# Performance work log

Measured on AMD Instinct MI355X. Metric: run time of the kernel, lower is better.

Reference implementation:

```python
import jax, jax.numpy as jnp
import numpy as np

EPS = 1e-12  # matches torch F.normalize eps
TEMPERATURE = 1.0
LAMBDA = 0.8


def _l2norm(x):
    n = jnp.sqrt(jnp.sum(x * x, axis=-1, keepdims=True))
    return x / jnp.maximum(n, EPS)


def setup_inputs() -> dict:
    key = jax.random.key(0)
    feats = jax.random.normal(key, (4, 4096, 512), dtype=jnp.float32)
    return {"feats": feats, "node": 8}


def reference(feats, node):
    f = _l2norm(feats)                                   # [B,N,D]
    scores = jnp.einsum('bnd,bmd->bnm', f, f) / TEMPERATURE  # [B,N,N]
    vals, idx = jax.lax.top_k(scores, node)              # [B,N,k]
    B, N, _ = scores.shape
    bi = jnp.arange(B)[:, None, None]
    ni = jnp.arange(N)[None, :, None]
    sparse = jnp.full_like(scores, -jnp.inf).at[bi, ni, idx].set(vals)
    w = jax.nn.softmax(sparse, axis=-1)                  # zeros outside top-k
    feats_att = jnp.einsum('bnm,bmd->bnd', w, f)
    feats_gam = f * LAMBDA + feats_att * (1.0 - LAMBDA)
    return _l2norm(feats_gam)
```

## Files before the change

### kernel.cpp

```cpp
#include <hip/hip_runtime.h>
#include <stdint.h>

#define NROWS 4096
#define NDIM  512
#define TOPT  8
#define NLIST 16
#define NCAND 128
#define NRESC 12
#define KSEL  8

typedef __attribute__((ext_vector_type(8))) short short8;
typedef __attribute__((ext_vector_type(4))) float f32x4;

__device__ __forceinline__ unsigned short f2bf(float x) {
  unsigned int u = __float_as_uint(x);
  return (unsigned short)((u + 0x7fffu + ((u >> 16) & 1u)) >> 16);
}

__device__ __forceinline__ void gl_lds16(const void* g, void* l) {
  void* gnc = (void*)g;
  __builtin_amdgcn_global_load_lds(
      (__attribute__((address_space(1))) void*)gnc,
      (__attribute__((address_space(3))) void*)l, 16, 0, 0);
}

__device__ __forceinline__ void ins8(unsigned int (&tv)[TOPT], unsigned int k) {
#pragma unroll
  for (int j = 0; j < TOPT; ++j) {
    const unsigned int nt = tv[j] > k ? tv[j] : k;
    k = tv[j] > k ? k : tv[j];
    tv[j] = nt;
  }
}

__global__ __launch_bounds__(256) void k_norm(const float* __restrict__ in,
                                              float* __restrict__ fout,
                                              unsigned short* __restrict__ fbf) {
  const int row = blockIdx.x * 4 + (threadIdx.x >> 6);
  const int l = threadIdx.x & 63;
  const float4* src = reinterpret_cast<const float4*>(in + (size_t)row * NDIM);
  float4 a = src[l * 2], b = src[l * 2 + 1];
  float ss = a.x * a.x + a.y * a.y + a.z * a.z + a.w * a.w +
             b.x * b.x + b.y * b.y + b.z * b.z + b.w * b.w;
#pragma unroll
  for (int off = 32; off; off >>= 1) ss += __shfl_xor(ss, off, 64);
  const float inv = 1.0f / fmaxf(sqrtf(ss), 1e-12f);
  a.x *= inv; a.y *= inv; a.z *= inv; a.w *= inv;
  b.x *= inv; b.y *= inv; b.z *= inv; b.w *= inv;
  float4* dst = reinterpret_cast<float4*>(fout + (size_t)row * NDIM);
  dst[l * 2] = a; dst[l * 2 + 1] = b;
  uint4 ub;
  ub.x = (unsigned)f2bf(a.x) | ((unsigned)f2bf(a.y) << 16);
  ub.y = (unsigned)f2bf(a.z) | ((unsigned)f2bf(a.w) << 16);
  ub.z = (unsigned)f2bf(b.x) | ((unsigned)f2bf(b.y) << 16);
  ub.w = (unsigned)f2bf(b.z) | ((unsigned)f2bf(b.w) << 16);
  reinterpret_cast<uint4*>(fbf + (size_t)row * NDIM)[l] = ub;
}

__global__ __launch_bounds__(512, 4) void k_coarse(const unsigned short* __restrict__ fbf,
                                                   unsigned int* __restrict__ keys) {
  __shared__ alignas(16) union {
    struct { unsigned short A[128 * 64]; unsigned short B[128 * 64]; } st;
    unsigned short S[128 * 128];
  } sh;

  const int tid = threadIdx.x;
  const int w = tid >> 6, l = tid & 63;

  const int lin = blockIdx.x;
  const int xcd = lin & 7;
  const int slot = lin >> 3;
  const int xq = xcd * 4 + (slot & 3);
  const int ym = (slot >> 2) & 7;
  const int zb = slot >> 5;

  const int q0 = xq * 128;
  const int m0 = ym * 512;
  const int bbase = zb * NROWS;

  const int qh = w >> 2, mq = w & 3;
  const int r = tid >> 2, sub = tid & 3;
  const int rx = r & 31;

  const int lrow = (l >> 3);
  const int lkg  = ((l & 7) ^ lrow) * 8;

  unsigned int tv[TOPT];
#pragma unroll
  for (int j = 0; j < TOPT; ++j) tv[j] = 0u;

  const f32x4 vzero = {0.f, 0.f, 0.f, 0.f};

  for (int mt = 0; mt < 4; ++mt) {
    const int mbase = m0 + mt * 128;
    f32x4 acc[4][2];
#pragma unroll
    for (int i = 0; i < 4; ++i)
#pragma unroll
      for (int j = 0; j < 2; ++j) acc[i][j] = vzero;

    for (int kt = 0; kt < 8; ++kt) {
      const int kk = kt * 64;
#pragma unroll
      for (int t = 0; t < 2; ++t) {
        const int sa = w * 2 + t;
        const int srow = sa * 8 + lrow;
        gl_lds16(fbf + ((size_t)(bbase + q0 + srow) << 9) + kk + lkg,
                 &sh.st.A[sa * 512]);
        gl_lds16(fbf + ((size_t)(bbase + mbase + srow) << 9) + kk + lkg,
                 &sh.st.B[sa * 512]);
      }
      __syncthreads();
#pragma unroll
      for (int ks = 0; ks < 2; ++ks) {
        short8 av[4], bv[2];
        const int kgrp = ks * 4 + (l >> 4);
#pragma unroll
        for (int i = 0; i < 4; ++i) {
          const int row = qh * 64 + i * 16 + (l & 15);
          av[i] = *(const short8*)&sh.st.A[row * 64 + (kgrp ^ (l & 7)) * 8];
        }
#pragma unroll
        for (int j = 0; j < 2; ++j) {
          const int row = mq * 32 + j * 16 + (l & 15);
          bv[j] = *(const short8*)&sh.st.B[row * 64 + (kgrp ^ (l & 7)) * 8];
        }
#pragma unroll
        for (int i = 0; i < 4; ++i)
#pragma unroll
          for (int j = 0; j < 2; ++j)
            acc[i][j] = __builtin_amdgcn_mfma_f32_16x16x32_bf16(av[i], bv[j], acc[i][j], 0, 0, 0);
      }
      __syncthreads();
    }

#pragma unroll
    for (int i = 0; i < 4; ++i) {
      const int qb_ = qh * 64 + i * 16 + (l >> 4) * 4;
#pragma unroll
      for (int j = 0; j < 2; ++j) {
        const int mc = mq * 32 + j * 16 + (l & 15);
#pragma unroll
        for (int rr = 0; rr < 4; ++rr) {
          const int q = qb_ + rr;
          unsigned int uu = __float_as_uint(acc[i][j][rr]);
          uu ^= (unsigned int)(((int)uu) >> 31) | 0x80000000u;
          const int pg = ((mc >> 2) ^ (q & 31));
          sh.S[q * 128 + pg * 4 + (mc & 3)] = (unsigned short)(uu >> 16);
        }
      }
    }
    __syncthreads();

    {
      const int invb0 = 4095 - (mbase + sub * 32);
#pragma unroll 4
      for (int cg = 0; cg < 8; ++cg) {
        const int pg = (sub * 8 + cg) ^ rx;
        const ushort4 s4 = *(const ushort4*)&sh.S[r * 128 + pg * 4];
        const unsigned int invb = (unsigned int)(invb0 - cg * 4);
        const unsigned int k0 = ((unsigned int)s4.x << 16) | invb;
        const unsigned int k1 = ((unsigned int)s4.y << 16) | (invb - 1);
        const unsigned int k2 = ((unsigned int)s4.z << 16) | (invb - 2);
        const unsigned int k3 = ((unsigned int)s4.w << 16) | (invb - 3);
        if (k0 > tv[TOPT - 1]) ins8(tv, k0);
        if (k1 > tv[TOPT - 1]) ins8(tv, k1);
        if (k2 > tv[TOPT - 1]) ins8(tv, k2);
        if (k3 > tv[TOPT - 1]) ins8(tv, k3);
      }
    }
    __syncthreads();
  }

  unsigned int ov[TOPT];
#pragma unroll
  for (int j = 0; j < TOPT; ++j) ov[j] = __shfl_xor(tv[j], 1, 64);
  unsigned int mg[TOPT];
#pragma unroll
  for (int j = 0; j < TOPT; ++j) {
    const unsigned int o = ov[TOPT - 1 - j];
    mg[j] = tv[j] > o ? tv[j] : o;
  }

  if ((sub & 1) == 0) {
    const int list = ym * 2 + (sub >> 1);
    unsigned int* dst = keys + (((size_t)(bbase + q0 + r)) * NLIST + list) * TOPT;
    reinterpret_cast<uint4*>(dst)[0] = make_uint4(mg[0], mg[1], mg[2], mg[3]);
    reinterpret_cast<uint4*>(dst)[1] = make_uint4(mg[4], mg[5], mg[6], mg[7]);
  }
}

__global__ __launch_bounds__(256) void k_sel(const float* __restrict__ f,
                                             const unsigned int* __restrict__ keys,
                                             uint2* __restrict__ selw) {
  __shared__ int sh_si[4][NRESC];

  const int lin = blockIdx.x;
  const int xcd = lin & 7;
  const int slot = lin >> 3;
  const int b = xcd >> 1;
  const int wv = threadIdx.x >> 6;
  const int n = ((xcd & 1) * 512 + slot) * 4 + wv;
  const int qg = b * NROWS + n;
  const int l = threadIdx.x & 63;

  const uint2 kk = reinterpret_cast<const uint2*>(keys + (size_t)qg * NCAND)[l];
  const unsigned int ka = kk.x, kb = kk.y;

  unsigned int T = 0u;
#pragma unroll
  for (int bit = 31; bit >= 0; --bit) {
    const unsigned int Tp = T | (1u << bit);
    const int cnt = (int)__popcll(__ballot(ka >= Tp)) +
                    (int)__popcll(__ballot(kb >= Tp));
    T = (cnt >= NRESC) ? Tp : T;
  }

  {
    const unsigned long long mA = __ballot(ka >= T);
    const unsigned long long mB = __ballot(kb >= T);
    const unsigned long long lt = (1ull << l) - 1ull;
    if (ka >= T) sh_si[wv][(int)__popcll(mA & lt)] = 4095 - (int)(ka & 4095u);
    if (kb >= T) sh_si[wv][(int)__popcll(mA) + (int)__popcll(mB & lt)] =
        4095 - (int)(kb & 4095u);
  }
  asm volatile("s_waitcnt lgkmcnt(0)" ::: "memory");
  __builtin_amdgcn_sched_barrier(0);

  int si[NRESC];
#pragma unroll
  for (int j = 0; j < NRESC; ++j)
    si[j] = __builtin_amdgcn_readfirstlane(sh_si[wv][j]);

  const float* __restrict__ fb = f + (size_t)b * NROWS * NDIM;
  const float* frow = fb + (size_t)n * NDIM;
  float selfv[8];
#pragma unroll
  for (int c = 0; c < 8; ++c) selfv[c] = frow[c * 64 + l];

  double ex[NRESC];
#pragma unroll
  for (int rr = 0; rr < NRESC; ++rr) {
    const float* g = fb + (size_t)si[rr] * NDIM;
    double s = 0.0;
#pragma unroll
    for (int c = 0; c < 8; ++c) s += (double)selfv[c] * (double)g[c * 64 + l];
    ex[rr] = s;
  }
#pragma unroll
  for (int off = 32; off; off >>= 1) {
#pragma unroll
    for (int rr = 0; rr < NRESC; ++rr) ex[rr] += __shfl_xor(ex[rr], off, 64);
  }

  unsigned mask = 0;
  double wex[KSEL]; int wi[KSEL];
#pragma unroll
  for (int rr = 0; rr < KSEL; ++rr) {
    double mv = -1.0e300; int midx = 0x7fffffff; int mslot = 0;
#pragma unroll
    for (int j = 0; j < NRESC; ++j) {
      const bool avail = ((mask >> j) & 1u) == 0u;
      if (avail && (ex[j] > mv || (ex[j] == mv && si[j] < midx))) {
        mv = ex[j]; midx = si[j]; mslot = j;
      }
    }
    mask |= 1u << mslot;
    wex[rr] = mv; wi[rr] = midx;
  }

  float w8[KSEL];
  const float mx = (float)wex[0];
  float wsum = 0.f;
#pragma unroll
  for (int rr = 0; rr < KSEL; ++rr) { w8[rr] = expf((float)wex[rr] - mx); wsum += w8[rr]; }
  const float cs = 0.2f / wsum;

  uint2 osel = make_uint2(0u, 0u);
#pragma unroll
  for (int rr = 0; rr < KSEL; ++rr) {
    if (l == rr) osel = make_uint2((unsigned)wi[rr], __float_as_uint(cs * w8[rr]));
  }
  if (l < KSEL) selw[(size_t)qg * KSEL + l] = osel;
}

__global__ __launch_bounds__(256) void k_blend(const float* __restrict__ f,
                                               const uint2* __restrict__ selw,
                                               float* __restrict__ out) {
  const int row = blockIdx.x * 4 + (threadIdx.x >> 6);
  const int b = row >> 12;
  const int l = threadIdx.x & 63;

  const uint2* pw = selw + (size_t)row * KSEL;
  uint2 p[KSEL];
#pragma unroll
  for (int j = 0; j < KSEL; ++j) p[j] = pw[j];

  const float* __restrict__ fb = f + (size_t)b * NROWS * NDIM;
  const float* frow = f + (size_t)row * NDIM;

  float acc[8];
#pragma unroll
  for (int c = 0; c < 8; ++c) acc[c] = 0.8f * frow[c * 64 + l];
#pragma unroll
  for (int j = 0; j < KSEL; ++j) {
    const float* g = fb + (size_t)p[j].x * NDIM;
    const float wr = __uint_as_float(p[j].y);
#pragma unroll
    for (int c = 0; c < 8; ++c) acc[c] = fmaf(wr, g[c * 64 + l], acc[c]);
  }

  float ss = 0.f;
#pragma unroll
  for (int c = 0; c < 8; ++c) ss += acc[c] * acc[c];
#pragma unroll
  for (int off = 32; off; off >>= 1) ss += __shfl_xor(ss, off, 64);
  const float inv = 1.0f / fmaxf(sqrtf(ss), 1e-12f);
  float* orow = out + (size_t)row * NDIM;
#pragma unroll
  for (int c = 0; c < 8; ++c) orow[c * 64 + l] = acc[c] * inv;
}

extern "C" void kernel_launch(void* const* d_in, const int* in_sizes, int n_in,
                              void* d_out, int out_size, void* d_ws, size_t ws_size,
                              hipStream_t stream) {
  (void)in_sizes; (void)n_in; (void)out_size; (void)ws_size;
  const float* feats = (const float*)d_in[0];
  char* ws = (char*)d_ws;
  float*          fnorm = (float*)(ws);
  unsigned short* fbf   = (unsigned short*)(ws + 33554432);
  unsigned int*   keys  = (unsigned int*)(ws + 50331648);
  uint2*          selw  = (uint2*)(ws + 58720256);
  float* out = (float*)d_out;

  k_norm <<<dim3(4096), dim3(256), 0, stream>>>(feats, fnorm, fbf);
  k_coarse<<<dim3(1024), dim3(512), 0, stream>>>(fbf, keys);
  k_sel  <<<dim3(4096), dim3(256), 0, stream>>>(fnorm, keys, selw);
  k_blend<<<dim3(4096), dim3(256), 0, stream>>>(fnorm, selw, out);
}
```

Measured before the change: 278.9 us.

## Exploit Gram symmetry: compute upper-triangle tiles only and drop fp32 normalized copy

The coarse scoring kernel now computes only the upper-triangular 128x128 tiles of each batch's symmetric similarity matrix. Each tile emits top-8 candidates for both its row block and its column block, using a transposed LDS copy, and diagonal tiles load a single operand. This roughly halves the bf16 MFMA work, but candidate lists double to 32 per row, so the selection kernel reads and radix-filters 256 keys instead of 128. The fp32 normalized feature buffer is also removed: later kernels re-read the raw input and multiply by a stored per-row inverse norm, saving a large write at the cost of extra multiplies and gathers.

New measurement: 246.7 us. 1.13x faster.

```diff
diff --git a/kernel.cpp b/kernel.cpp
--- a/kernel.cpp
+++ b/kernel.cpp
@@ -3,9 +3,11 @@
 
 #define NROWS 4096
 #define NDIM  512
+#define NTILE 32
+#define NPAIR 528
 #define TOPT  8
-#define NLIST 16
-#define NCAND 128
+#define NLIST 32
+#define NCAND 256
 #define NRESC 12
 #define KSEL  8
 
@@ -33,9 +35,29 @@
   }
 }
 
+__device__ __forceinline__ void ce_desc(unsigned int& x, unsigned int& y) {
+  const unsigned int hi = x > y ? x : y, lo = x > y ? y : x;
+  x = hi; y = lo;
+}
+__device__ __forceinline__ void bitonic8_desc(unsigned int (&a)[TOPT]) {
+  ce_desc(a[0], a[4]); ce_desc(a[1], a[5]); ce_desc(a[2], a[6]); ce_desc(a[3], a[7]);
+  ce_desc(a[0], a[2]); ce_desc(a[1], a[3]); ce_desc(a[4], a[6]); ce_desc(a[5], a[7]);
+  ce_desc(a[0], a[1]); ce_desc(a[2], a[3]); ce_desc(a[4], a[5]); ce_desc(a[6], a[7]);
+}
+__device__ __forceinline__ void xormerge(unsigned int (&a)[TOPT], int xm) {
+  unsigned int ov[TOPT];
+#pragma unroll
+  for (int j = 0; j < TOPT; ++j) ov[j] = __shfl_xor(a[j], xm, 64);
+  unsigned int r[TOPT];
+#pragma unroll
+  for (int j = 0; j < TOPT; ++j) r[j] = a[j] > ov[TOPT - 1 - j] ? a[j] : ov[TOPT - 1 - j];
+#pragma unroll
+  for (int j = 0; j < TOPT; ++j) a[j] = r[j];
+}
+
 __global__ __launch_bounds__(256) void k_norm(const float* __restrict__ in,
-                                              float* __restrict__ fout,
-                                              unsigned short* __restrict__ fbf) {
+                                              unsigned short* __restrict__ fbf,
+                                              float* __restrict__ invn) {
   const int row = blockIdx.x * 4 + (threadIdx.x >> 6);
   const int l = threadIdx.x & 63;
   const float4* src = reinterpret_cast<const float4*>(in + (size_t)row * NDIM);
@@ -45,10 +67,9 @@
 #pragma unroll
   for (int off = 32; off; off >>= 1) ss += __shfl_xor(ss, off, 64);
   const float inv = 1.0f / fmaxf(sqrtf(ss), 1e-12f);
+  if (l == 0) invn[row] = inv;
   a.x *= inv; a.y *= inv; a.z *= inv; a.w *= inv;
   b.x *= inv; b.y *= inv; b.z *= inv; b.w *= inv;
-  float4* dst = reinterpret_cast<float4*>(fout + (size_t)row * NDIM);
-  dst[l * 2] = a; dst[l * 2 + 1] = b;
   uint4 ub;
   ub.x = (unsigned)f2bf(a.x) | ((unsigned)f2bf(a.y) << 16);
   ub.y = (unsigned)f2bf(a.z) | ((unsigned)f2bf(a.w) << 16);
@@ -59,24 +80,28 @@
 
 __global__ __launch_bounds__(512, 4) void k_coarse(const unsigned short* __restrict__ fbf,
                                                    unsigned int* __restrict__ keys) {
-  __shared__ alignas(16) union {
-    struct { unsigned short A[128 * 64]; unsigned short B[128 * 64]; } st;
-    unsigned short S[128 * 128];
+  __shared__ alignas(16) struct {
+    union {
+      struct { unsigned short A[128 * 64]; unsigned short B[128 * 64]; } st;
+      unsigned short S[128 * 128];
+    } u;
+    unsigned short T[128 * 128];
   } sh;
 
   const int tid = threadIdx.x;
   const int w = tid >> 6, l = tid & 63;
 
   const int lin = blockIdx.x;
-  const int xcd = lin & 7;
-  const int slot = lin >> 3;
-  const int xq = xcd * 4 + (slot & 3);
-  const int ym = (slot >> 2) & 7;
-  const int zb = slot >> 5;
-
-  const int q0 = xq * 128;
-  const int m0 = ym * 512;
+  const int zb = lin / NPAIR;
+  int rem = lin - zb * NPAIR;
+  int ti = 0;
+  while (rem >= NTILE - ti) { rem -= NTILE - ti; ++ti; }
+  const int tj = ti + rem;
+
+  const int q0 = ti * 128;
+  const int m0 = tj * 128;
   const int bbase = zb * NROWS;
+  const bool diag = (ti == tj);
 
   const int qh = w >> 2, mq = w & 3;
   const int r = tid >> 2, sub = tid & 3;
@@ -85,112 +110,132 @@
   const int lrow = (l >> 3);
   const int lkg  = ((l & 7) ^ lrow) * 8;
 
-  unsigned int tv[TOPT];
-#pragma unroll
-  for (int j = 0; j < TOPT; ++j) tv[j] = 0u;
-
   const f32x4 vzero = {0.f, 0.f, 0.f, 0.f};
-
-  for (int mt = 0; mt < 4; ++mt) {
-    const int mbase = m0 + mt * 128;
-    f32x4 acc[4][2];
-#pragma unroll
-    for (int i = 0; i < 4; ++i)
-#pragma unroll
-      for (int j = 0; j < 2; ++j) acc[i][j] = vzero;
-
-    for (int kt = 0; kt < 8; ++kt) {
-      const int kk = kt * 64;
-#pragma unroll
-      for (int t = 0; t < 2; ++t) {
-        const int sa = w * 2 + t;
-        const int srow = sa * 8 + lrow;
-        gl_lds16(fbf + ((size_t)(bbase + q0 + srow) << 9) + kk + lkg,
-                 &sh.st.A[sa * 512]);
-        gl_lds16(fbf + ((size_t)(bbase + mbase + srow) << 9) + kk + lkg,
-                 &sh.st.B[sa * 512]);
+  f32x4 acc[4][2];
+#pragma unroll
+  for (int i = 0; i < 4; ++i)
+#pragma unroll
+    for (int j = 0; j < 2; ++j) acc[i][j] = vzero;
+
+  for (int kt = 0; kt < 8; ++kt) {
+    const int kk = kt * 64;
+#pragma unroll
+    for (int t = 0; t < 2; ++t) {
+      const int sa = w * 2 + t;
+      const int srow = sa * 8 + lrow;
+      gl_lds16(fbf + ((size_t)(bbase + q0 + srow) << 9) + kk + lkg,
+               &sh.u.st.A[sa * 512]);
+      if (!diag)
+        gl_lds16(fbf + ((size_t)(bbase + m0 + srow) << 9) + kk + lkg,
+                 &sh.u.st.B[sa * 512]);
+    }
+    __syncthreads();
+    const unsigned short* Bb = diag ? sh.u.st.A : sh.u.st.B;
+#pragma unroll
+    for (int ks = 0; ks < 2; ++ks) {
+      short8 av[4], bv[2];
+      const int kgrp = ks * 4 + (l >> 4);
+#pragma unroll
+      for (int i = 0; i < 4; ++i) {
+        const int row = qh * 64 + i * 16 + (l & 15);
+        av[i] = *(const short8*)&sh.u.st.A[row * 64 + (kgrp ^ (l & 7)) * 8];
       }
-      __syncthreads();
-#pragma unroll
-      for (int ks = 0; ks < 2; ++ks) {
-        short8 av[4], bv[2];
-        const int kgrp = ks * 4 + (l >> 4);
-#pragma unroll
-        for (int i = 0; i < 4; ++i) {
-          const int row = qh * 64 + i * 16 + (l & 15);
-          av[i] = *(const short8*)&sh.st.A[row * 64 + (kgrp ^ (l & 7)) * 8];
-        }
-#pragma unroll
-        for (int j = 0; j < 2; ++j) {
-          const int row = mq * 32 + j * 16 + (l & 15);
-          bv[j] = *(const short8*)&sh.st.B[row * 64 + (kgrp ^ (l & 7)) * 8];
-        }
-#pragma unroll
-        for (int i = 0; i < 4; ++i)
-#pragma unroll
-          for (int j = 0; j < 2; ++j)
-            acc[i][j] = __builtin_amdgcn_mfma_f32_16x16x32_bf16(av[i], bv[j], acc[i][j], 0, 0, 0);
+#pragma unroll
+      for (int j = 0; j < 2; ++j) {
+        const int row = mq * 32 + j * 16 + (l & 15);
+        bv[j] = *(const short8*)&Bb[row * 64 + (kgrp ^ (l & 7)) * 8];
       }
-      __syncthreads();
-    }
-
-#pragma unroll
-    for (int i = 0; i < 4; ++i) {
-      const int qb_ = qh * 64 + i * 16 + (l >> 4) * 4;
-#pragma unroll
-      for (int j = 0; j < 2; ++j) {
-        const int mc = mq * 32 + j * 16 + (l & 15);
-#pragma unroll
-        for (int rr = 0; rr < 4; ++rr) {
-          const int q = qb_ + rr;
-          unsigned int uu = __float_as_uint(acc[i][j][rr]);
-          uu ^= (unsigned int)(((int)uu) >> 31) | 0x80000000u;
-          const int pg = ((mc >> 2) ^ (q & 31));
-          sh.S[q * 128 + pg * 4 + (mc & 3)] = (unsigned short)(uu >> 16);
-        }
+#pragma unroll
+      for (int i = 0; i < 4; ++i)
+#pragma unroll
+        for (int j = 0; j < 2; ++j)
+          acc[i][j] = __builtin_amdgcn_mfma_f32_16x16x32_bf16(av[i], bv[j], acc[i][j], 0, 0, 0);
+    }
+    __syncthreads();
+  }
+
+#pragma unroll
+  for (int i = 0; i < 4; ++i) {
+    const int qb_ = qh * 64 + i * 16 + (l >> 4) * 4;
+#pragma unroll
+    for (int j = 0; j < 2; ++j) {
+      const int mc = mq * 32 + j * 16 + (l & 15);
+#pragma unroll
+      for (int rr = 0; rr < 4; ++rr) {
+        const int q = qb_ + rr;
+        unsigned int uu = __float_as_uint(acc[i][j][rr]);
+        uu ^= (unsigned int)(((int)uu) >> 31) | 0x80000000u;
+        const unsigned short k16 = (unsigned short)(uu >> 16);
+        const int pg = ((mc >> 2) ^ (q & 31));
+        sh.u.S[q * 128 + pg * 4 + (mc & 3)] = k16;
+        const int pgt = ((q >> 2) ^ (mc & 31));
+        sh.T[mc * 128 + pgt * 4 + (q & 3)] = k16;
       }
     }
-    __syncthreads();
-
-    {
-      const int invb0 = 4095 - (mbase + sub * 32);
-#pragma unroll 4
-      for (int cg = 0; cg < 8; ++cg) {
-        const int pg = (sub * 8 + cg) ^ rx;
-        const ushort4 s4 = *(const ushort4*)&sh.S[r * 128 + pg * 4];
-        const unsigned int invb = (unsigned int)(invb0 - cg * 4);
-        const unsigned int k0 = ((unsigned int)s4.x << 16) | invb;
-        const unsigned int k1 = ((unsigned int)s4.y << 16) | (invb - 1);
-        const unsigned int k2 = ((unsigned int)s4.z << 16) | (invb - 2);
-        const unsigned int k3 = ((unsigned int)s4.w << 16) | (invb - 3);
-        if (k0 > tv[TOPT - 1]) ins8(tv, k0);
-        if (k1 > tv[TOPT - 1]) ins8(tv, k1);
-        if (k2 > tv[TOPT - 1]) ins8(tv, k2);
-        if (k3 > tv[TOPT - 1]) ins8(tv, k3);
-      }
-    }
-    __syncthreads();
-  }
-
-  unsigned int ov[TOPT];
-#pragma unroll
-  for (int j = 0; j < TOPT; ++j) ov[j] = __shfl_xor(tv[j], 1, 64);
-  unsigned int mg[TOPT];
-#pragma unroll
-  for (int j = 0; j < TOPT; ++j) {
-    const unsigned int o = ov[TOPT - 1 - j];
-    mg[j] = tv[j] > o ? tv[j] : o;
-  }
-
-  if ((sub & 1) == 0) {
-    const int list = ym * 2 + (sub >> 1);
-    unsigned int* dst = keys + (((size_t)(bbase + q0 + r)) * NLIST + list) * TOPT;
-    reinterpret_cast<uint4*>(dst)[0] = make_uint4(mg[0], mg[1], mg[2], mg[3]);
-    reinterpret_cast<uint4*>(dst)[1] = make_uint4(mg[4], mg[5], mg[6], mg[7]);
-  }
-}
-
-__global__ __launch_bounds__(256) void k_sel(const float* __restrict__ f,
+  }
+  __syncthreads();
+
+  {
+    unsigned int tv[TOPT];
+#pragma unroll
+    for (int j = 0; j < TOPT; ++j) tv[j] = 0u;
+    const int invb0 = 4095 - (m0 + sub * 32);
+#pragma unroll
+    for (int cg = 0; cg < 8; ++cg) {
+      const int pg = (sub * 8 + cg) ^ rx;
+      const ushort4 s4 = *(const ushort4*)&sh.u.S[r * 128 + pg * 4];
+      const unsigned int invb = (unsigned int)(invb0 - cg * 4);
+      const unsigned int k0 = ((unsigned int)s4.x << 16) | invb;
+      const unsigned int k1 = ((unsigned int)s4.y << 16) | (invb - 1);
+      const unsigned int k2 = ((unsigned int)s4.z << 16) | (invb - 2);
+      const unsigned int k3 = ((unsigned int)s4.w << 16) | (invb - 3);
+      if (k0 > tv[TOPT - 1]) ins8(tv, k0);
+      if (k1 > tv[TOPT - 1]) ins8(tv, k1);
+      if (k2 > tv[TOPT - 1]) ins8(tv, k2);
+      if (k3 > tv[TOPT - 1]) ins8(tv, k3);
+    }
+    xormerge(tv, 1);
+    bitonic8_desc(tv);
+    xormerge(tv, 2);
+    if (sub == 0) {
+      unsigned int* dst = keys + (((size_t)(bbase + q0 + r)) * NLIST + tj) * TOPT;
+      reinterpret_cast<uint4*>(dst)[0] = make_uint4(tv[0], tv[1], tv[2], tv[3]);
+      reinterpret_cast<uint4*>(dst)[1] = make_uint4(tv[4], tv[5], tv[6], tv[7]);
+    }
+  }
+
+  if (!diag) {
+    unsigned int tv[TOPT];
+#pragma unroll
+    for (int j = 0; j < TOPT; ++j) tv[j] = 0u;
+    const int invb0 = 4095 - (q0 + sub * 32);
+#pragma unroll
+    for (int cg = 0; cg < 8; ++cg) {
+      const int pg = (sub * 8 + cg) ^ rx;
+      const ushort4 s4 = *(const ushort4*)&sh.T[r * 128 + pg * 4];
+      const unsigned int invb = (unsigned int)(invb0 - cg * 4);
+      const unsigned int k0 = ((unsigned int)s4.x << 16) | invb;
+      const unsigned int k1 = ((unsigned int)s4.y << 16) | (invb - 1);
+      const unsigned int k2 = ((unsigned int)s4.z << 16) | (invb - 2);
+      const unsigned int k3 = ((unsigned int)s4.w << 16) | (invb - 3);
+      if (k0 > tv[TOPT - 1]) ins8(tv, k0);
+      if (k1 > tv[TOPT - 1]) ins8(tv, k1);
+      if (k2 > tv[TOPT - 1]) ins8(tv, k2);
+      if (k3 > tv[TOPT - 1]) ins8(tv, k3);
+    }
+    xormerge(tv, 1);
+    bitonic8_desc(tv);
+    xormerge(tv, 2);
+    if (sub == 0) {
+      unsigned int* dst = keys + (((size_t)(bbase + m0 + r)) * NLIST + ti) * TOPT;
+      reinterpret_cast<uint4*>(dst)[0] = make_uint4(tv[0], tv[1], tv[2], tv[3]);
+      reinterpret_cast<uint4*>(dst)[1] = make_uint4(tv[4], tv[5], tv[6], tv[7]);
+    }
+  }
+}
+
+__global__ __launch_bounds__(256) void k_sel(const float* __restrict__ feats,
+                                             const float* __restrict__ invn,
                                              const unsigned int* __restrict__ keys,
                                              uint2* __restrict__ selw) {
   __shared__ int sh_si[4][NRESC];
@@ -204,25 +249,33 @@
   const int qg = b * NROWS + n;
   const int l = threadIdx.x & 63;
 
-  const uint2 kk = reinterpret_cast<const uint2*>(keys + (size_t)qg * NCAND)[l];
-  const unsigned int ka = kk.x, kb = kk.y;
+  const uint4 kv = reinterpret_cast<const uint4*>(keys + (size_t)qg * NCAND)[l];
+  const unsigned int ka = kv.x, kb = kv.y, kc = kv.z, kd = kv.w;
 
   unsigned int T = 0u;
 #pragma unroll
   for (int bit = 31; bit >= 0; --bit) {
     const unsigned int Tp = T | (1u << bit);
     const int cnt = (int)__popcll(__ballot(ka >= Tp)) +
-                    (int)__popcll(__ballot(kb >= Tp));
+                    (int)__popcll(__ballot(kb >= Tp)) +
+                    (int)__popcll(__ballot(kc >= Tp)) +
+                    (int)__popcll(__ballot(kd >= Tp));
     T = (cnt >= NRESC) ? Tp : T;
   }
 
   {
     const unsigned long long mA = __ballot(ka >= T);
     const unsigned long long mB = __ballot(kb >= T);
+    const unsigned long long mC = __ballot(kc >= T);
+    const unsigned long long mD = __ballot(kd >= T);
     const unsigned long long lt = (1ull << l) - 1ull;
+    const int oB = (int)__popcll(mA);
+    const int oC = oB + (int)__popcll(mB);
+    const int oD = oC + (int)__popcll(mC);
     if (ka >= T) sh_si[wv][(int)__popcll(mA & lt)] = 4095 - (int)(ka & 4095u);
-    if (kb >= T) sh_si[wv][(int)__popcll(mA) + (int)__popcll(mB & lt)] =
-        4095 - (int)(kb & 4095u);
+    if (kb >= T) sh_si[wv][oB + (int)__popcll(mB & lt)] = 4095 - (int)(kb & 4095u);
+    if (kc >= T) sh_si[wv][oC + (int)__popcll(mC & lt)] = 4095 - (int)(kc & 4095u);
+    if (kd >= T) sh_si[wv][oD + (int)__popcll(mD & lt)] = 4095 - (int)(kd & 4095u);
   }
   asm volatile("s_waitcnt lgkmcnt(0)" ::: "memory");
   __builtin_amdgcn_sched_barrier(0);
@@ -232,19 +285,22 @@
   for (int j = 0; j < NRESC; ++j)
     si[j] = __builtin_amdgcn_readfirstlane(sh_si[wv][j]);
 
-  const float* __restrict__ fb = f + (size_t)b * NROWS * NDIM;
+  const float* __restrict__ fb = feats + (size_t)b * NROWS * NDIM;
   const float* frow = fb + (size_t)n * NDIM;
+  const float ia = invn[qg];
   float selfv[8];
 #pragma unroll
-  for (int c = 0; c < 8; ++c) selfv[c] = frow[c * 64 + l];
+  for (int c = 0; c < 8; ++c) selfv[c] = frow[c * 64 + l] * ia;
 
   double ex[NRESC];
 #pragma unroll
   for (int rr = 0; rr < NRESC; ++rr) {
     const float* g = fb + (size_t)si[rr] * NDIM;
+    const float ib = invn[b * NROWS + si[rr]];
     double s = 0.0;
 #pragma unroll
-    for (int c = 0; c < 8; ++c) s += (double)selfv[c] * (double)g[c * 64 + l];
+    for (int c = 0; c < 8; ++c)
+      s += (double)selfv[c] * (double)(g[c * 64 + l] * ib);
     ex[rr] = s;
   }
 #pragma unroll
@@ -284,7 +340,8 @@
   if (l < KSEL) selw[(size_t)qg * KSEL + l] = osel;
 }
 
-__global__ __launch_bounds__(256) void k_blend(const float* __restrict__ f,
+__global__ __launch_bounds__(256) void k_blend(const float* __restrict__ feats,
+                                               const float* __restrict__ invn,
                                                const uint2* __restrict__ selw,
                                                float* __restrict__ out) {
   const int row = blockIdx.x * 4 + (threadIdx.x >> 6);
@@ -296,18 +353,20 @@
 #pragma unroll
   for (int j = 0; j < KSEL; ++j) p[j] = pw[j];
 
-  const float* __restrict__ fb = f + (size_t)b * NROWS * NDIM;
-  const float* frow = f + (size_t)row * NDIM;
+  const float* __restrict__ fb = feats + (size_t)b * NROWS * NDIM;
+  const float* frow = feats + (size_t)row * NDIM;
+  const float ia = invn[row];
 
   float acc[8];
 #pragma unroll
-  for (int c = 0; c < 8; ++c) acc[c] = 0.8f * frow[c * 64 + l];
+  for (int c = 0; c < 8; ++c) acc[c] = 0.8f * (frow[c * 64 + l] * ia);
 #pragma unroll
   for (int j = 0; j < KSEL; ++j) {
     const float* g = fb + (size_t)p[j].x * NDIM;
+    const float ib = invn[b * NROWS + (int)p[j].x];
     const float wr = __uint_as_float(p[j].y);
 #pragma unroll
-    for (int c = 0; c < 8; ++c) acc[c] = fmaf(wr, g[c * 64 + l], acc[c]);
+    for (int c = 0; c < 8; ++c) acc[c] = fmaf(wr, g[c * 64 + l] * ib, acc[c]);
   }
 
   float ss = 0.f;
@@ -327,14 +386,14 @@
   (void)in_sizes; (void)n_in; (void)out_size; (void)ws_size;
   const float* feats = (const float*)d_in[0];
   char* ws = (char*)d_ws;
-  float*          fnorm = (float*)(ws);
-  unsigned short* fbf   = (unsigned short*)(ws + 33554432);
-  unsigned int*   keys  = (unsigned int*)(ws + 50331648);
-  uint2*          selw  = (uint2*)(ws + 58720256);
+  unsigned short* fbf  = (unsigned short*)(ws);
+  unsigned int*   keys = (unsigned int*)(ws + 16777216);
+  float*          invn = (float*)(ws + 33554432);
+  uint2*          selw = (uint2*)(ws + 33619968);
   float* out = (float*)d_out;
 
-  k_norm <<<dim3(4096), dim3(256), 0, stream>>>(feats, fnorm, fbf);
-  k_coarse<<<dim3(1024), dim3(512), 0, stream>>>(fbf, keys);
-  k_sel  <<<dim3(4096), dim3(256), 0, stream>>>(fnorm, keys, selw);
-  k_blend<<<dim3(4096), dim3(256), 0, stream>>>(fnorm, selw, out);
-}
+  k_norm  <<<dim3(4096), dim3(256), 0, stream>>>(feats, fbf, invn);
+  k_coarse<<<dim3(4 * NPAIR), dim3(512), 0, stream>>>(fbf, keys);
+  k_sel   <<<dim3(4096), dim3(256), 0, stream>>>(feats, invn, keys, selw);
+  k_blend <<<dim3(4096), dim3(256), 0, stream>>>(feats, invn, selw, out);
+}
```
